# Performance work log

Measured on AMD Instinct MI355X. Metric: run time of the kernel, lower is better.

## Reference

```python
import jax, jax.numpy as jnp
import numpy as np

SHIFT = 1  # module picks shift_direction in {-1,+1} at init via random(); fixed to +1


def setup_inputs() -> dict:
    key = jax.random.key(0)
    kx, kw = jax.random.split(key)
    x = jax.random.normal(kx, (128, 128, 28, 28), dtype=jnp.float32)  # (B, Cin, H, W)
    w = jax.random.normal(kw, (32, 128, 3), dtype=jnp.float32)        # (Cout, Cin, K)
    return {"x": x, "w": w}


def reference(x, w):
    # The unfold+einsum in the original is a conv1d over the last (W) axis with
    # kernel 3, padding 1; the H axis is untouched. Express it as a 2D conv with
    # a (1,3) kernel so no im2col buffer is materialized.
    y = jax.lax.conv_general_dilated(
        x, w[:, :, None, :],                     # kernel (Cout, Cin, 1, 3)
        window_strides=(1, 1),
        padding=((0, 0), (1, 1)),
        dimension_numbers=("NCHW", "OIHW", "NCHW"))  # -> (B, 32, H, W)
    # Original rolls the H axis (after moving it next to batch) by shift_direction.
    return jnp.roll(y, SHIFT, axis=2)
```

## Files before the change

kernel.cpp:

```cpp
#include <hip/hip_runtime.h>


#define CIN  128
#define COUT 32
#define HH   28
#define WW   28
#define CIP  136
#define WPD  34

typedef __attribute__((ext_vector_type(8))) short short8;
typedef __attribute__((ext_vector_type(8))) __bf16 bf16x8;
typedef __attribute__((ext_vector_type(16))) float f32x16;

__device__ inline unsigned short f2bf(float f) {
    union { float f; unsigned u; } v; v.f = f;
    return (unsigned short)((v.u + 0x7FFFu + ((v.u >> 16) & 1u)) >> 16);
}

__global__ void build_wfrag(const float* __restrict__ wt, unsigned short* __restrict__ wf) {
    int t = blockIdx.x * 256 + threadIdx.x;
    if (t >= 24 * 64 * 8) return;
    int j = t & 7, lane = (t >> 3) & 63, s = t >> 9;
    int co = lane & 31;
    int k  = s * 16 + (lane >> 5) * 8 + j;
    int kk = k >> 7, ci = k & 127;
    wf[t] = f2bf(wt[((size_t)co * CIN + ci) * 3 + kk]);
}

__global__ __launch_bounds__(256) void conv_mfma(
    const float* __restrict__ x,
    const unsigned short* __restrict__ wf,
    float* __restrict__ out)
{
    __shared__ __align__(16) unsigned short xt[4][WPD][CIP];

    const int tid = threadIdx.x;
    const int hq  = blockIdx.x;
    const int b   = blockIdx.y;
    const int h0  = hq * 4;
    const float* xb = x + (size_t)b * CIN * HH * WW;

    for (int i = tid; i < 4 * 6 * CIP; i += 256) {
        int ci = i % CIP; int q = i / CIP;
        int wsel = q % 6, hl = q / 6;
        int wp = (wsel == 0) ? 0 : 28 + wsel;
        xt[hl][wp][ci] = 0;
    }

#pragma unroll
    for (int it = 0; it < 14; ++it) {
        int idx  = tid + it * 256;
        int w4   = idx % 7;
        int rest = idx / 7;
        int hl   = rest & 3;
        int ci   = rest >> 2;
        float4 v = *(const float4*)(xb + ((size_t)ci * HH + (h0 + hl)) * WW + w4 * 4);
        int wp = 1 + w4 * 4;
        xt[hl][wp + 0][ci] = f2bf(v.x);
        xt[hl][wp + 1][ci] = f2bf(v.y);
        xt[hl][wp + 2][ci] = f2bf(v.z);
        xt[hl][wp + 3][ci] = f2bf(v.w);
    }

    const int lane = tid & 63;
    const int hl   = tid >> 6;
    short8 afr[24];
#pragma unroll
    for (int s = 0; s < 24; ++s)
        afr[s] = *(const short8*)(wf + (size_t)(s * 64 + lane) * 8);

    __syncthreads();

    const int n    = lane & 31;
    const int half = lane >> 5;
    f32x16 acc = {0,0,0,0,0,0,0,0,0,0,0,0,0,0,0,0};

#pragma unroll
    for (int s = 0; s < 24; ++s) {
        int kk  = s >> 3;
        int cib = (s & 7) * 16 + half * 8;
        short8 bfr = *(const short8*)&xt[hl][n + kk][cib];
        acc = __builtin_amdgcn_mfma_f32_32x32x16_bf16(
            __builtin_bit_cast(bf16x8, afr[s]),
            __builtin_bit_cast(bf16x8, bfr), acc, 0, 0, 0);
    }

    if (n < WW) {
        const int hout = (h0 + hl + 1) % HH;
#pragma unroll
        for (int r = 0; r < 16; ++r) {
            int co = (r & 3) + 8 * (r >> 2) + 4 * half;
            out[(((size_t)b * COUT + co) * HH + hout) * WW + n] = acc[r];
        }
    }
}

extern "C" void kernel_launch(void* const* d_in, const int* in_sizes, int n_in,
                              void* d_out, int out_size, void* d_ws, size_t ws_size,
                              hipStream_t stream) {
    const float* x  = (const float*)d_in[0];
    const float* wt = (const float*)d_in[1];
    float* out = (float*)d_out;
    unsigned short* wf = (unsigned short*)d_ws;

    build_wfrag<<<48, 256, 0, stream>>>(wt, wf);
    dim3 grid(HH / 4, 128);
    conv_mfma<<<grid, 256, 0, stream>>>(x, wf, out);
}
```

Measured before the change: 93.50 us.

## Halve rows per block, stream weight fragments per tap, raise occupancy

Each block now handles 2 H rows with 128 threads instead of 4 rows with 256, which doubles the grid to 14x128 blocks and halves LDS use per block. Weight fragments are loaded in three groups of 8 per kernel tap instead of all 24 up front, cutting register pressure, and launch bounds ask for 4 blocks per CU. Pad zeroing now uses 32-bit stores and the load loop is only partially unrolled. The aim is more resident waves to hide global-load latency, at the cost of more blocks each re-reading the weight fragments.

```diff
diff --git a/kernel.cpp b/kernel.cpp
--- a/kernel.cpp
+++ b/kernel.cpp
@@ -1,12 +1,14 @@
 #include <hip/hip_runtime.h>
 
 
-#define CIN  128
-#define COUT 32
-#define HH   28
-#define WW   28
-#define CIP  136
-#define WPD  34
+#define CIN   128
+#define COUT  32
+#define HH    28
+#define WW    28
+#define CIP   136
+#define WPD   34
+#define HROWS 2
+#define NTHR  128
 
 typedef __attribute__((ext_vector_type(8))) short short8;
 typedef __attribute__((ext_vector_type(8))) __bf16 bf16x8;
@@ -27,33 +29,38 @@
     wf[t] = f2bf(wt[((size_t)co * CIN + ci) * 3 + kk]);
 }
 
-__global__ __launch_bounds__(256) void conv_mfma(
+__global__ __launch_bounds__(NTHR, 4) void conv_mfma(
     const float* __restrict__ x,
     const unsigned short* __restrict__ wf,
     float* __restrict__ out)
 {
-    __shared__ __align__(16) unsigned short xt[4][WPD][CIP];
+    __shared__ __align__(16) unsigned short xt[HROWS][WPD][CIP];
 
     const int tid = threadIdx.x;
-    const int hq  = blockIdx.x;
+    const int hp  = blockIdx.x;
     const int b   = blockIdx.y;
-    const int h0  = hq * 4;
+    const int h0  = hp * HROWS;
     const float* xb = x + (size_t)b * CIN * HH * WW;
 
-    for (int i = tid; i < 4 * 6 * CIP; i += 256) {
-        int ci = i % CIP; int q = i / CIP;
-        int wsel = q % 6, hl = q / 6;
-        int wp = (wsel == 0) ? 0 : 28 + wsel;
-        xt[hl][wp][ci] = 0;
+    {
+        unsigned int* xu = (unsigned int*)xt;
+        const int ROWU = CIP / 2;
+        const int HU   = WPD * ROWU;
+        for (int i = tid; i < HROWS * 6 * ROWU; i += NTHR) {
+            int hl  = i / (6 * ROWU);
+            int r   = i - hl * (6 * ROWU);
+            int off = (r < ROWU) ? r : (29 * ROWU + (r - ROWU));
+            xu[hl * HU + off] = 0u;
+        }
     }
 
-#pragma unroll
+#pragma unroll 2
     for (int it = 0; it < 14; ++it) {
-        int idx  = tid + it * 256;
+        int idx  = tid + it * NTHR;
         int w4   = idx % 7;
         int rest = idx / 7;
-        int hl   = rest & 3;
-        int ci   = rest >> 2;
+        int hl   = rest & (HROWS - 1);
+        int ci   = rest >> 1;
         float4 v = *(const float4*)(xb + ((size_t)ci * HH + (h0 + hl)) * WW + w4 * 4);
         int wp = 1 + w4 * 4;
         xt[hl][wp + 0][ci] = f2bf(v.x);
@@ -62,27 +69,27 @@
         xt[hl][wp + 3][ci] = f2bf(v.w);
     }
 
+    __syncthreads();
+
     const int lane = tid & 63;
     const int hl   = tid >> 6;
-    short8 afr[24];
-#pragma unroll
-    for (int s = 0; s < 24; ++s)
-        afr[s] = *(const short8*)(wf + (size_t)(s * 64 + lane) * 8);
-
-    __syncthreads();
-
     const int n    = lane & 31;
     const int half = lane >> 5;
     f32x16 acc = {0,0,0,0,0,0,0,0,0,0,0,0,0,0,0,0};
 
 #pragma unroll
-    for (int s = 0; s < 24; ++s) {
-        int kk  = s >> 3;
-        int cib = (s & 7) * 16 + half * 8;
-        short8 bfr = *(const short8*)&xt[hl][n + kk][cib];
-        acc = __builtin_amdgcn_mfma_f32_32x32x16_bf16(
-            __builtin_bit_cast(bf16x8, afr[s]),
-            __builtin_bit_cast(bf16x8, bfr), acc, 0, 0, 0);
+    for (int kk = 0; kk < 3; ++kk) {
+        short8 afr[8];
+#pragma unroll
+        for (int u = 0; u < 8; ++u)
+            afr[u] = *(const short8*)(wf + (size_t)((kk * 8 + u) * 64 + lane) * 8);
+#pragma unroll
+        for (int u = 0; u < 8; ++u) {
+            short8 bfr = *(const short8*)&xt[hl][n + kk][u * 16 + half * 8];
+            acc = __builtin_amdgcn_mfma_f32_32x32x16_bf16(
+                __builtin_bit_cast(bf16x8, afr[u]),
+                __builtin_bit_cast(bf16x8, bfr), acc, 0, 0, 0);
+        }
     }
 
     if (n < WW) {
@@ -104,6 +111,6 @@
     unsigned short* wf = (unsigned short*)d_ws;
 
     build_wfrag<<<48, 256, 0, stream>>>(wt, wf);
-    dim3 grid(HH / 4, 128);
-    conv_mfma<<<grid, 256, 0, stream>>>(x, wf, out);
+    dim3 grid(HH / HROWS, 128);
+    conv_mfma<<<grid, NTHR, 0, stream>>>(x, wf, out);
 }
```

New measurement: 95.00 us. No clear change (+1.6%).
